# Kernel optimization log

Measured on AMD Instinct MI355X. Metric: run time of the kernel, lower is better.

The kernel has to match this reference:

```python
import jax, jax.numpy as jnp
import numpy as np

L1 = 256
INPUTS = 41024
FACTOR_INPUTS = 64
B = 2048


def setup_inputs() -> dict:
    key = jax.random.key(0)
    k_us, k_them, k_w, k_b, k_W, k_bias = jax.random.split(key, 6)
    us = jax.random.uniform(k_us, (B, 1), dtype=jnp.float32)
    them = jax.random.uniform(k_them, (B, 1), dtype=jnp.float32)
    w_in = jax.random.uniform(k_w, (B, INPUTS), dtype=jnp.float32)
    b_in = jax.random.uniform(k_b, (B, INPUTS), dtype=jnp.float32)
    # Linear weight [L1, INPUTS]; last FACTOR_INPUTS columns zeroed as in __init__
    W = jax.random.normal(k_W, (L1, INPUTS), dtype=jnp.float32) * 0.01
    W = W.at[:, INPUTS - FACTOR_INPUTS:].set(0.0)
    bias = jax.random.normal(k_bias, (L1,), dtype=jnp.float32) * 0.01
    return {"us": us, "them": them, "w_in": w_in, "b_in": b_in, "W": W, "bias": bias}


def reference(us, them, w_in, b_in, W, bias):
    # sparse-feature linear (dense reference): [B, INPUTS] @ [INPUTS, L1]
    w = jnp.dot(w_in, W.T) + bias          # [B, L1]
    b = jnp.dot(b_in, W.T) + bias          # [B, L1]
    wb = jnp.concatenate([w, b], axis=1)   # [B, 2*L1]
    bw = jnp.concatenate([b, w], axis=1)   # [B, 2*L1]
    l0 = us * wb + them * bw               # perspective mix
    return jnp.clip(l0, 0.0, 1.0)          # Hardtanh(0, 1) == clipped relu
```

## Files before the change

kernel.cpp:

```cpp
#include <hip/hip_runtime.h>
#include <stdint.h>

#define C_INPUTS 41024
#define C_KEFF   40960
#define C_L1     256
#define C_BATCH  2048
#define C_BK     32
#define C_MTILE  64
#define C_KSPLIT 8
#define C_KCHUNK (C_KEFF / C_KSPLIT)
#define C_NITER  (C_KCHUNK / C_BK)
#define C_MBLOCKS 64
#define C_NKT    (C_KEFF / C_BK)
#define C_WTILE  (C_L1 * C_BK * 2)
#define C_ATILE  (C_MTILE * C_BK * 2)
#define C_BUF    (C_WTILE + C_ATILE)
#define C_NBUF   3
#define LDS_TOTAL (C_NBUF * C_BUF)
#define WS_W_BYTES ((size_t)C_L1 * C_KEFF * 2)

typedef __attribute__((ext_vector_type(8))) short  short8;
typedef __attribute__((ext_vector_type(4))) float  f32x4;

typedef __attribute__((address_space(1))) const uint32_t g_as1_u32;
typedef __attribute__((address_space(3))) uint32_t      l_as3_u32;

__device__ __forceinline__ uint16_t bf16_rtne(float f) {
  uint32_t u = __builtin_bit_cast(uint32_t, f);
  u += 0x7fffu + ((u >> 16) & 1u);
  return (uint16_t)(u >> 16);
}

__global__ __launch_bounds__(256) void k_convert_w(const float* __restrict__ W,
                                                   uint16_t* __restrict__ wsW) {
  const int kt = blockIdx.x;
  const int t  = threadIdx.x;
  const int l  = t & 63;
  const int fb = t >> 6;
  const int rm = l & 15;
  const int kg = l >> 4;
  const int kcol = kt * C_BK + kg * 8;
  uint16_t* dst = wsW + (size_t)kt * (C_L1 * C_BK) + (size_t)l * 8;
#pragma unroll
  for (int q = 0; q < 4; ++q) {
    const int f = fb * 4 + q;
    const int row = f * 16 + rm;
    const float4* s = (const float4*)(W + (size_t)row * C_INPUTS + kcol);
    float4 x = s[0];
    float4 y = s[1];
    union { uint16_t h[8]; short8 v; } u;
    u.h[0] = bf16_rtne(x.x); u.h[1] = bf16_rtne(x.y);
    u.h[2] = bf16_rtne(x.z); u.h[3] = bf16_rtne(x.w);
    u.h[4] = bf16_rtne(y.x); u.h[5] = bf16_rtne(y.y);
    u.h[6] = bf16_rtne(y.z); u.h[7] = bf16_rtne(y.w);
    *(short8*)(dst + (size_t)f * 512) = u.v;
  }
}

__global__ __launch_bounds__(256, 2) void k_gemm(const float* __restrict__ w_in,
                                                 const float* __restrict__ b_in,
                                                 const uint16_t* __restrict__ wsW,
                                                 float* __restrict__ wsP) {
  extern __shared__ char smem[];
  const int bid  = blockIdx.x;
  const int ks   = bid & 7;
  const int mb   = bid >> 3;
  const int tid  = threadIdx.x;
  const int wave = tid >> 6;
  const int lane = tid & 63;
  const int lrow = lane & 15;
  const int lg   = lane >> 4;

  const int k0 = ks * C_KCHUNK;
  const float* Abase = (mb < 32)
      ? (w_in + (size_t)mb * C_MTILE * C_INPUTS)
      : (b_in + (size_t)(mb - 32) * C_MTILE * C_INPUTS);

  const int ar = tid >> 2;
  const int ac = tid & 3;
  const float* aptr = Abase + (size_t)ar * C_INPUTS + k0 + ac * 8;
  const int awoff = C_WTILE + ((ar >> 4) << 10) + ((ac * 16 + (ar & 15)) << 4);

  const char* wg = (const char*)wsW + (size_t)(ks * C_NITER) * C_WTILE
                 + (size_t)wave * 4096 + (size_t)lane * 16;

  f32x4 acc[4][4];
#pragma unroll
  for (int i = 0; i < 4; ++i)
#pragma unroll
    for (int j = 0; j < 4; ++j) acc[i][j] = (f32x4){0.f, 0.f, 0.f, 0.f};

  float4 avA[2], avB[2];
  int cb = 0;

  {
#pragma unroll
    for (int c = 0; c < 4; ++c) {
      __builtin_amdgcn_global_load_lds((g_as1_u32*)(wg + c * 1024),
                                       (l_as3_u32*)(smem + wave * 4096 + c * 1024), 16, 0, 0);
      __builtin_amdgcn_global_load_lds((g_as1_u32*)(wg + C_WTILE + c * 1024),
                                       (l_as3_u32*)(smem + C_BUF + wave * 4096 + c * 1024), 16, 0, 0);
    }
    const float4* p0 = (const float4*)aptr;
    avA[0] = p0[0]; avA[1] = p0[1];
    const float4* p1 = (const float4*)(aptr + C_BK);
    avB[0] = p1[0]; avB[1] = p1[1];
    union { uint16_t h[8]; short8 v; } u;
    u.h[0] = bf16_rtne(avA[0].x); u.h[1] = bf16_rtne(avA[0].y);
    u.h[2] = bf16_rtne(avA[0].z); u.h[3] = bf16_rtne(avA[0].w);
    u.h[4] = bf16_rtne(avA[1].x); u.h[5] = bf16_rtne(avA[1].y);
    u.h[6] = bf16_rtne(avA[1].z); u.h[7] = bf16_rtne(avA[1].w);
    *(short8*)(smem + awoff) = u.v;
    asm volatile("s_waitcnt vmcnt(0)" ::: "memory");
    asm volatile("s_waitcnt lgkmcnt(0)" ::: "memory");
    __builtin_amdgcn_s_barrier();
    __builtin_amdgcn_sched_barrier(0);
  }

#define GEMM_STEP(T, AVI, AVC) do {                                          \
    const bool pf = (T) + 2 < C_NITER;                                       \
    const int nb1 = (cb + C_BUF < LDS_TOTAL) ? cb + C_BUF : cb + C_BUF - LDS_TOTAL; \
    const int nb2 = (nb1 + C_BUF < LDS_TOTAL) ? nb1 + C_BUF : nb1 + C_BUF - LDS_TOTAL; \
    if (pf) {                                                                \
      const float4* p = (const float4*)(aptr + (size_t)((T) + 2) * C_BK);    \
      AVI[0] = p[0]; AVI[1] = p[1];                                          \
      const char* wsrc = wg + (size_t)((T) + 2) * C_WTILE;                   \
      char* wdst = smem + nb2 + wave * 4096;                                 \
      _Pragma("unroll")                                                      \
      for (int c = 0; c < 4; ++c)                                            \
        __builtin_amdgcn_global_load_lds((g_as1_u32*)(wsrc + c * 1024),      \
                                         (l_as3_u32*)(wdst + c * 1024), 16, 0, 0); \
    }                                                                        \
    {                                                                        \
      const char* ab = smem + cb;                                            \
      short8 af[4], bf[4];                                                   \
      _Pragma("unroll")                                                      \
      for (int mi = 0; mi < 4; ++mi)                                         \
        af[mi] = *(const short8*)(ab + C_WTILE + mi * 1024 + lane * 16);     \
      _Pragma("unroll")                                                      \
      for (int ni = 0; ni < 4; ++ni)                                         \
        bf[ni] = *(const short8*)(ab + wave * 4096 + ni * 1024 + lane * 16); \
      _Pragma("unroll")                                                      \
      for (int mi = 0; mi < 4; ++mi)                                         \
        _Pragma("unroll")                                                    \
        for (int ni = 0; ni < 4; ++ni)                                       \
          acc[mi][ni] = __builtin_amdgcn_mfma_f32_16x16x32_bf16(af[mi], bf[ni], acc[mi][ni], 0, 0, 0); \
    }                                                                        \
    if ((T) + 1 < C_NITER) {                                                 \
      union { uint16_t h[8]; short8 v; } u;                                  \
      u.h[0] = bf16_rtne(AVC[0].x); u.h[1] = bf16_rtne(AVC[0].y);            \
      u.h[2] = bf16_rtne(AVC[0].z); u.h[3] = bf16_rtne(AVC[0].w);            \
      u.h[4] = bf16_rtne(AVC[1].x); u.h[5] = bf16_rtne(AVC[1].y);            \
      u.h[6] = bf16_rtne(AVC[1].z); u.h[7] = bf16_rtne(AVC[1].w);            \
      *(short8*)(smem + nb1 + awoff) = u.v;                                  \
    }                                                                        \
    if (pf) { asm volatile("s_waitcnt vmcnt(6)" ::: "memory"); }             \
    else    { asm volatile("s_waitcnt vmcnt(0)" ::: "memory"); }             \
    asm volatile("s_waitcnt lgkmcnt(0)" ::: "memory");                       \
    __builtin_amdgcn_s_barrier();                                            \
    __builtin_amdgcn_sched_barrier(0);                                       \
    cb = nb1;                                                                \
  } while (0)

#pragma unroll 1
  for (int t = 0; t < C_NITER; t += 2) {
    GEMM_STEP(t,     avA, avB);
    GEMM_STEP(t + 1, avB, avA);
  }
#undef GEMM_STEP

  float* P = wsP + ((size_t)ks * 4096 + (size_t)mb * C_MTILE) * 256;
#pragma unroll
  for (int mi = 0; mi < 4; ++mi)
#pragma unroll
    for (int ni = 0; ni < 4; ++ni)
#pragma unroll
      for (int j = 0; j < 4; ++j) {
        const int rr = mi * 16 + lg * 4 + j;
        const int cc = wave * 64 + ni * 16 + lrow;
        P[(size_t)rr * 256 + cc] = acc[mi][ni][j];
      }
}

__global__ __launch_bounds__(256) void k_reduce(const float* __restrict__ wsP,
                                                const float* __restrict__ us,
                                                const float* __restrict__ them,
                                                const float* __restrict__ bias,
                                                float* __restrict__ out) {
  const int r = blockIdx.x;
  const int c = threadIdx.x;
  float wd = 0.f, bd = 0.f;
#pragma unroll
  for (int s = 0; s < C_KSPLIT; ++s) {
    wd += wsP[((size_t)s * 4096 + r) * 256 + c];
    bd += wsP[((size_t)s * 4096 + 2048 + r) * 256 + c];
  }
  const float bi = bias[c];
  const float w = wd + bi;
  const float b = bd + bi;
  const float u = us[r];
  const float t = them[r];
  float o1 = u * w + t * b;
  float o2 = u * b + t * w;
  o1 = fminf(fmaxf(o1, 0.f), 1.f);
  o2 = fminf(fmaxf(o2, 0.f), 1.f);
  out[(size_t)r * 512 + c]       = o1;
  out[(size_t)r * 512 + 256 + c] = o2;
}

extern "C" void kernel_launch(void* const* d_in, const int* in_sizes, int n_in,
                              void* d_out, int out_size, void* d_ws, size_t ws_size,
                              hipStream_t stream) {
  const float* us   = (const float*)d_in[0];
  const float* them = (const float*)d_in[1];
  const float* w_in = (const float*)d_in[2];
  const float* b_in = (const float*)d_in[3];
  const float* W    = (const float*)d_in[4];
  const float* bias = (const float*)d_in[5];
  float* out = (float*)d_out;

  uint16_t* wsW = (uint16_t*)d_ws;
  float*    wsP = (float*)((char*)d_ws + WS_W_BYTES);

  k_convert_w<<<C_NKT, 256, 0, stream>>>(W, wsW);
  k_gemm<<<C_MBLOCKS * C_KSPLIT, 256, LDS_TOTAL, stream>>>(w_in, b_in, wsW, wsP);
  k_reduce<<<C_BATCH, 256, 0, stream>>>(wsP, us, them, bias, out);
}
```

Measured before the change: 220.7 us.

## Load bf16 weights directly to registers, shrink LDS to A-only, raise K-split

The GEMM no longer stages the pre-converted bf16 weight tile through LDS with global_load_lds. Each wave now loads its weight fragments straight into registers and only the converted activation tile is double-buffered in a small static LDS array, processed 64 K per step. Occupancy hint goes to 3 blocks per CU, and K-split rises to 16 when the workspace allows, giving 1024 blocks. The aim is to cut LDS traffic and footprint and add parallelism, at the cost of doubling partial-sum writes and reduce reads, and of exposing global weight-load latency with less prefetch depth.

```diff
diff --git a/kernel.cpp b/kernel.cpp
--- a/kernel.cpp
+++ b/kernel.cpp
@@ -4,31 +4,25 @@
 #define C_INPUTS 41024
 #define C_KEFF   40960
 #define C_L1     256
-#define C_BATCH  2048
-#define C_BK     32
-#define C_MTILE  64
-#define C_KSPLIT 8
-#define C_KCHUNK (C_KEFF / C_KSPLIT)
-#define C_NITER  (C_KCHUNK / C_BK)
-#define C_MBLOCKS 64
-#define C_NKT    (C_KEFF / C_BK)
-#define C_WTILE  (C_L1 * C_BK * 2)
-#define C_ATILE  (C_MTILE * C_BK * 2)
-#define C_BUF    (C_WTILE + C_ATILE)
-#define C_NBUF   3
-#define LDS_TOTAL (C_NBUF * C_BUF)
+#define C_NT32   (C_KEFF / 32)
 #define WS_W_BYTES ((size_t)C_L1 * C_KEFF * 2)
 
-typedef __attribute__((ext_vector_type(8))) short  short8;
-typedef __attribute__((ext_vector_type(4))) float  f32x4;
-
-typedef __attribute__((address_space(1))) const uint32_t g_as1_u32;
-typedef __attribute__((address_space(3))) uint32_t      l_as3_u32;
+typedef __attribute__((ext_vector_type(8))) short short8;
+typedef __attribute__((ext_vector_type(4))) float f32x4;
 
 __device__ __forceinline__ uint16_t bf16_rtne(float f) {
   uint32_t u = __builtin_bit_cast(uint32_t, f);
   u += 0x7fffu + ((u >> 16) & 1u);
   return (uint16_t)(u >> 16);
+}
+
+__device__ __forceinline__ short8 pack_bf16x8(float4 a, float4 b) {
+  union { uint16_t h[8]; short8 v; } u;
+  u.h[0] = bf16_rtne(a.x); u.h[1] = bf16_rtne(a.y);
+  u.h[2] = bf16_rtne(a.z); u.h[3] = bf16_rtne(a.w);
+  u.h[4] = bf16_rtne(b.x); u.h[5] = bf16_rtne(b.y);
+  u.h[6] = bf16_rtne(b.z); u.h[7] = bf16_rtne(b.w);
+  return u.v;
 }
 
 __global__ __launch_bounds__(256) void k_convert_w(const float* __restrict__ W,
@@ -39,50 +33,46 @@
   const int fb = t >> 6;
   const int rm = l & 15;
   const int kg = l >> 4;
-  const int kcol = kt * C_BK + kg * 8;
-  uint16_t* dst = wsW + (size_t)kt * (C_L1 * C_BK) + (size_t)l * 8;
+  const int kcol = kt * 32 + kg * 8;
+  uint16_t* dst = wsW + (size_t)kt * (C_L1 * 32) + (size_t)l * 8;
 #pragma unroll
   for (int q = 0; q < 4; ++q) {
     const int f = fb * 4 + q;
     const int row = f * 16 + rm;
     const float4* s = (const float4*)(W + (size_t)row * C_INPUTS + kcol);
-    float4 x = s[0];
-    float4 y = s[1];
-    union { uint16_t h[8]; short8 v; } u;
-    u.h[0] = bf16_rtne(x.x); u.h[1] = bf16_rtne(x.y);
-    u.h[2] = bf16_rtne(x.z); u.h[3] = bf16_rtne(x.w);
-    u.h[4] = bf16_rtne(y.x); u.h[5] = bf16_rtne(y.y);
-    u.h[6] = bf16_rtne(y.z); u.h[7] = bf16_rtne(y.w);
-    *(short8*)(dst + (size_t)f * 512) = u.v;
-  }
-}
-
-__global__ __launch_bounds__(256, 2) void k_gemm(const float* __restrict__ w_in,
+    *(short8*)(dst + (size_t)f * 512) = pack_bf16x8(s[0], s[1]);
+  }
+}
+
+template<int KSPLIT>
+__global__ __launch_bounds__(256, 3) void k_gemm(const float* __restrict__ w_in,
                                                  const float* __restrict__ b_in,
                                                  const uint16_t* __restrict__ wsW,
                                                  float* __restrict__ wsP) {
-  extern __shared__ char smem[];
+  constexpr int KCHUNK = C_KEFF / KSPLIT;
+  constexpr int NITER  = KCHUNK / 64;
+  __shared__ short8 abuf[2][512];
+
   const int bid  = blockIdx.x;
-  const int ks   = bid & 7;
-  const int mb   = bid >> 3;
+  const int ks   = bid % KSPLIT;
+  const int mb   = bid / KSPLIT;
   const int tid  = threadIdx.x;
   const int wave = tid >> 6;
   const int lane = tid & 63;
   const int lrow = lane & 15;
   const int lg   = lane >> 4;
 
-  const int k0 = ks * C_KCHUNK;
-  const float* Abase = (mb < 32)
-      ? (w_in + (size_t)mb * C_MTILE * C_INPUTS)
-      : (b_in + (size_t)(mb - 32) * C_MTILE * C_INPUTS);
-
+  const float* Abase = (mb < 32) ? (w_in + (size_t)mb * 64 * C_INPUTS)
+                                 : (b_in + (size_t)(mb - 32) * 64 * C_INPUTS);
   const int ar = tid >> 2;
   const int ac = tid & 3;
-  const float* aptr = Abase + (size_t)ar * C_INPUTS + k0 + ac * 8;
-  const int awoff = C_WTILE + ((ar >> 4) << 10) + ((ac * 16 + (ar & 15)) << 4);
-
-  const char* wg = (const char*)wsW + (size_t)(ks * C_NITER) * C_WTILE
-                 + (size_t)wave * 4096 + (size_t)lane * 16;
+  const float* aptr = Abase + (size_t)ar * C_INPUTS + ks * KCHUNK + ac * 8;
+
+  const int slot0 = (ar >> 4) * 64 + ac * 16 + (ar & 15);
+  const int slot1 = slot0 + 256;
+
+  const uint16_t* wbase = wsW + (size_t)(ks * (KCHUNK / 32)) * 8192
+                        + wave * 2048 + lane * 8;
 
   f32x4 acc[4][4];
 #pragma unroll
@@ -90,98 +80,82 @@
 #pragma unroll
     for (int j = 0; j < 4; ++j) acc[i][j] = (f32x4){0.f, 0.f, 0.f, 0.f};
 
-  float4 avA[2], avB[2];
-  int cb = 0;
-
-  {
-#pragma unroll
-    for (int c = 0; c < 4; ++c) {
-      __builtin_amdgcn_global_load_lds((g_as1_u32*)(wg + c * 1024),
-                                       (l_as3_u32*)(smem + wave * 4096 + c * 1024), 16, 0, 0);
-      __builtin_amdgcn_global_load_lds((g_as1_u32*)(wg + C_WTILE + c * 1024),
-                                       (l_as3_u32*)(smem + C_BUF + wave * 4096 + c * 1024), 16, 0, 0);
-    }
-    const float4* p0 = (const float4*)aptr;
-    avA[0] = p0[0]; avA[1] = p0[1];
-    const float4* p1 = (const float4*)(aptr + C_BK);
-    avB[0] = p1[0]; avB[1] = p1[1];
-    union { uint16_t h[8]; short8 v; } u;
-    u.h[0] = bf16_rtne(avA[0].x); u.h[1] = bf16_rtne(avA[0].y);
-    u.h[2] = bf16_rtne(avA[0].z); u.h[3] = bf16_rtne(avA[0].w);
-    u.h[4] = bf16_rtne(avA[1].x); u.h[5] = bf16_rtne(avA[1].y);
-    u.h[6] = bf16_rtne(avA[1].z); u.h[7] = bf16_rtne(avA[1].w);
-    *(short8*)(smem + awoff) = u.v;
-    asm volatile("s_waitcnt vmcnt(0)" ::: "memory");
-    asm volatile("s_waitcnt lgkmcnt(0)" ::: "memory");
-    __builtin_amdgcn_s_barrier();
-    __builtin_amdgcn_sched_barrier(0);
-  }
-
-#define GEMM_STEP(T, AVI, AVC) do {                                          \
-    const bool pf = (T) + 2 < C_NITER;                                       \
-    const int nb1 = (cb + C_BUF < LDS_TOTAL) ? cb + C_BUF : cb + C_BUF - LDS_TOTAL; \
-    const int nb2 = (nb1 + C_BUF < LDS_TOTAL) ? nb1 + C_BUF : nb1 + C_BUF - LDS_TOTAL; \
-    if (pf) {                                                                \
-      const float4* p = (const float4*)(aptr + (size_t)((T) + 2) * C_BK);    \
-      AVI[0] = p[0]; AVI[1] = p[1];                                          \
-      const char* wsrc = wg + (size_t)((T) + 2) * C_WTILE;                   \
-      char* wdst = smem + nb2 + wave * 4096;                                 \
-      _Pragma("unroll")                                                      \
-      for (int c = 0; c < 4; ++c)                                            \
-        __builtin_amdgcn_global_load_lds((g_as1_u32*)(wsrc + c * 1024),      \
-                                         (l_as3_u32*)(wdst + c * 1024), 16, 0, 0); \
-    }                                                                        \
-    {                                                                        \
-      const char* ab = smem + cb;                                            \
-      short8 af[4], bf[4];                                                   \
-      _Pragma("unroll")                                                      \
-      for (int mi = 0; mi < 4; ++mi)                                         \
-        af[mi] = *(const short8*)(ab + C_WTILE + mi * 1024 + lane * 16);     \
-      _Pragma("unroll")                                                      \
-      for (int ni = 0; ni < 4; ++ni)                                         \
-        bf[ni] = *(const short8*)(ab + wave * 4096 + ni * 1024 + lane * 16); \
-      _Pragma("unroll")                                                      \
-      for (int mi = 0; mi < 4; ++mi)                                         \
-        _Pragma("unroll")                                                    \
-        for (int ni = 0; ni < 4; ++ni)                                       \
-          acc[mi][ni] = __builtin_amdgcn_mfma_f32_16x16x32_bf16(af[mi], bf[ni], acc[mi][ni], 0, 0, 0); \
-    }                                                                        \
-    if ((T) + 1 < C_NITER) {                                                 \
-      union { uint16_t h[8]; short8 v; } u;                                  \
-      u.h[0] = bf16_rtne(AVC[0].x); u.h[1] = bf16_rtne(AVC[0].y);            \
-      u.h[2] = bf16_rtne(AVC[0].z); u.h[3] = bf16_rtne(AVC[0].w);            \
-      u.h[4] = bf16_rtne(AVC[1].x); u.h[5] = bf16_rtne(AVC[1].y);            \
-      u.h[6] = bf16_rtne(AVC[1].z); u.h[7] = bf16_rtne(AVC[1].w);            \
-      *(short8*)(smem + nb1 + awoff) = u.v;                                  \
-    }                                                                        \
-    if (pf) { asm volatile("s_waitcnt vmcnt(6)" ::: "memory"); }             \
-    else    { asm volatile("s_waitcnt vmcnt(0)" ::: "memory"); }             \
-    asm volatile("s_waitcnt lgkmcnt(0)" ::: "memory");                       \
-    __builtin_amdgcn_s_barrier();                                            \
-    __builtin_amdgcn_sched_barrier(0);                                       \
-    cb = nb1;                                                                \
+  float4 aA[4], aB[4];
+  short8 wX[4], wY[4];
+
+#define LOAD_A(DST, T) do {                                    \
+    const float* p_ = aptr + (size_t)(T) * 64;                 \
+    DST[0] = ((const float4*)p_)[0];                           \
+    DST[1] = ((const float4*)p_)[1];                           \
+    DST[2] = ((const float4*)(p_ + 32))[0];                    \
+    DST[3] = ((const float4*)(p_ + 32))[1];                    \
+  } while (0)
+
+#define LOAD_W(DST, TILE) do {                                 \
+    const uint16_t* q_ = wbase + (size_t)(TILE) * 8192;        \
+    DST[0] = *(const short8*)(q_);                             \
+    DST[1] = *(const short8*)(q_ + 512);                       \
+    DST[2] = *(const short8*)(q_ + 1024);                      \
+    DST[3] = *(const short8*)(q_ + 1536);                      \
+  } while (0)
+
+#define CVT_WRITE(SRC, BUF) do {                               \
+    abuf[BUF][slot0] = pack_bf16x8(SRC[0], SRC[1]);            \
+    abuf[BUF][slot1] = pack_bf16x8(SRC[2], SRC[3]);            \
+  } while (0)
+
+  LOAD_A(aA, 0);
+  LOAD_A(aB, 1);
+  LOAD_W(wX, 0);
+  CVT_WRITE(aA, 0);
+  __syncthreads();
+
+#define STEP(T, AVI, AVC) do {                                                  \
+    const int buf_ = (T) & 1;                                                   \
+    if ((T) + 2 < NITER) LOAD_A(AVI, (T) + 2);                                  \
+    short8 af_[4];                                                              \
+    _Pragma("unroll") for (int mi = 0; mi < 4; ++mi)                            \
+      af_[mi] = abuf[buf_][mi * 64 + lane];                                     \
+    LOAD_W(wY, 2 * (T) + 1);                                                    \
+    _Pragma("unroll") for (int mi = 0; mi < 4; ++mi)                            \
+      _Pragma("unroll") for (int nj = 0; nj < 4; ++nj)                          \
+        acc[mi][nj] = __builtin_amdgcn_mfma_f32_16x16x32_bf16(af_[mi], wX[nj],  \
+                                                              acc[mi][nj], 0, 0, 0); \
+    _Pragma("unroll") for (int mi = 0; mi < 4; ++mi)                            \
+      af_[mi] = abuf[buf_][256 + mi * 64 + lane];                               \
+    if ((T) + 1 < NITER) LOAD_W(wX, 2 * (T) + 2);                               \
+    _Pragma("unroll") for (int mi = 0; mi < 4; ++mi)                            \
+      _Pragma("unroll") for (int nj = 0; nj < 4; ++nj)                          \
+        acc[mi][nj] = __builtin_amdgcn_mfma_f32_16x16x32_bf16(af_[mi], wY[nj],  \
+                                                              acc[mi][nj], 0, 0, 0); \
+    if ((T) + 1 < NITER) CVT_WRITE(AVC, buf_ ^ 1);                              \
+    __syncthreads();                                                            \
   } while (0)
 
 #pragma unroll 1
-  for (int t = 0; t < C_NITER; t += 2) {
-    GEMM_STEP(t,     avA, avB);
-    GEMM_STEP(t + 1, avB, avA);
-  }
-#undef GEMM_STEP
-
-  float* P = wsP + ((size_t)ks * 4096 + (size_t)mb * C_MTILE) * 256;
+  for (int t = 0; t < NITER; t += 2) {
+    STEP(t,     aA, aB);
+    STEP(t + 1, aB, aA);
+  }
+#undef STEP
+#undef LOAD_A
+#undef LOAD_W
+#undef CVT_WRITE
+
+  float* P = wsP + ((size_t)ks * 4096 + (size_t)mb * 64) * 256;
 #pragma unroll
   for (int mi = 0; mi < 4; ++mi)
 #pragma unroll
-    for (int ni = 0; ni < 4; ++ni)
+    for (int nj = 0; nj < 4; ++nj)
 #pragma unroll
       for (int j = 0; j < 4; ++j) {
         const int rr = mi * 16 + lg * 4 + j;
-        const int cc = wave * 64 + ni * 16 + lrow;
-        P[(size_t)rr * 256 + cc] = acc[mi][ni][j];
+        const int cc = wave * 64 + nj * 16 + lrow;
+        P[(size_t)rr * 256 + cc] = acc[mi][nj][j];
       }
 }
 
+template<int KSPLIT>
 __global__ __launch_bounds__(256) void k_reduce(const float* __restrict__ wsP,
                                                 const float* __restrict__ us,
                                                 const float* __restrict__ them,
@@ -191,7 +165,7 @@
   const int c = threadIdx.x;
   float wd = 0.f, bd = 0.f;
 #pragma unroll
-  for (int s = 0; s < C_KSPLIT; ++s) {
+  for (int s = 0; s < KSPLIT; ++s) {
     wd += wsP[((size_t)s * 4096 + r) * 256 + c];
     bd += wsP[((size_t)s * 4096 + 2048 + r) * 256 + c];
   }
@@ -222,7 +196,14 @@
   uint16_t* wsW = (uint16_t*)d_ws;
   float*    wsP = (float*)((char*)d_ws + WS_W_BYTES);
 
-  k_convert_w<<<C_NKT, 256, 0, stream>>>(W, wsW);
-  k_gemm<<<C_MBLOCKS * C_KSPLIT, 256, LDS_TOTAL, stream>>>(w_in, b_in, wsW, wsP);
-  k_reduce<<<C_BATCH, 256, 0, stream>>>(wsP, us, them, bias, out);
-}
+  k_convert_w<<<C_NT32, 256, 0, stream>>>(W, wsW);
+
+  const size_t need16 = WS_W_BYTES + (size_t)16 * 4096 * 256 * 4;
+  if (ws_size >= need16) {
+    k_gemm<16><<<64 * 16, 256, 0, stream>>>(w_in, b_in, wsW, wsP);
+    k_reduce<16><<<2048, 256, 0, stream>>>(wsP, us, them, bias, out);
+  } else {
+    k_gemm<8><<<64 * 8, 256, 0, stream>>>(w_in, b_in, wsW, wsP);
+    k_reduce<8><<<2048, 256, 0, stream>>>(wsP, us, them, bias, out);
+  }
+}
```

After: 262.4 us. +18.9%, slower.
